# Performance work log

Hardware: AMD Instinct MI355X
Metric: run time of the kernel (lower is better)

## Reference

```python
import jax, jax.numpy as jnp
import numpy as np

N = 1024      # nodes (fully connected graph -> N^2 edges)
D = 3         # spatial dim
H_DIM = 64    # node feature dim
MSG = 64      # edge message dim
HID = 128     # MLP hidden dim


def _linear_init(key, fan_in, fan_out):
    k1, k2 = jax.random.split(key)
    s = 1.0 / np.sqrt(fan_in)
    w = jax.random.uniform(k1, (fan_in, fan_out), minval=-s, maxval=s, dtype=jnp.float32)
    b = jax.random.uniform(k2, (fan_out,), minval=-s, maxval=s, dtype=jnp.float32)
    return w, b


def setup_inputs() -> dict:
    key = jax.random.key(0)
    kx, kh, ke1, ke2, kn1, kn2, kc1, kc2 = jax.random.split(key, 8)
    x = jax.random.normal(kx, (N, D), dtype=jnp.float32)
    h = jax.random.normal(kh, (N, H_DIM), dtype=jnp.float32)
    # edge_mlp: (2*h_dim + 1) -> HID -> MSG
    ew1, eb1 = _linear_init(ke1, 2 * H_DIM + 1, HID)
    ew2, eb2 = _linear_init(ke2, HID, MSG)
    # node_mlp: (h_dim + msg) -> HID -> h_dim
    nw1, nb1 = _linear_init(kn1, H_DIM + MSG, HID)
    nw2, nb2 = _linear_init(kn2, HID, H_DIM)
    # coord_mlp: msg -> HID -> 1
    cw1, cb1 = _linear_init(kc1, MSG, HID)
    cw2, cb2 = _linear_init(kc2, HID, 1)
    return {"x": x, "h": h,
            "ew1": ew1, "eb1": eb1, "ew2": ew2, "eb2": eb2,
            "nw1": nw1, "nb1": nb1, "nw2": nw2, "nb2": nb2,
            "cw1": cw1, "cb1": cb1, "cw2": cw2, "cb2": cb2}


def _mlp2(inp, w1, b1, w2, b2):
    # depth-2 MLP: Linear -> SiLU -> Linear (no output activation)
    return jax.nn.silu(inp @ w1 + b1) @ w2 + b2


def reference(x, h, ew1, eb1, ew2, eb2, nw1, nb1, nw2, nb2, cw1, cb1, cw2, cb2):
    n = x.shape[0]
    # pairwise displacement and squared distance: (N,N,D), (N,N,1)
    dx = x[:, None, :] - x[None, :, :]
    r2 = jnp.sum(dx * dx, axis=-1, keepdims=True)
    hd = h.shape[-1]
    h_i = jnp.broadcast_to(h[:, None, :], (n, n, hd))
    h_j = jnp.broadcast_to(h[None, :, :], (n, n, hd))
    edge_in = jnp.concatenate([h_i, h_j, r2], axis=-1)      # (N,N,2H+1)
    m_ij = _mlp2(edge_in, ew1, eb1, ew2, eb2)               # (N,N,MSG)
    not_self = 1.0 - jnp.eye(n, dtype=x.dtype)
    m_ij = m_ij * not_self[:, :, None]
    phi_ij = _mlp2(m_ij, cw1, cb1, cw2, cb2)                # (N,N,1)
    x_update = jnp.sum(dx * phi_ij, axis=1) / (n - 1 + 1e-08)
    x_new = x + x_update
    m_i = jnp.sum(m_ij, axis=1)                             # (N,MSG)
    node_in = jnp.concatenate([h, m_i], axis=-1)            # (N,H+MSG)
    dh = _mlp2(node_in, nw1, nb1, nw2, nb2)                 # (N,H)
    h_new = h + dh  # residual_h = True
    return (x_new, h_new)
```

## Files before the change

### kernel.cpp

```cpp
#include <hip/hip_runtime.h>
#include <hip/hip_bf16.h>

#define NN   1024
#define HD   64
#define MSGD 64
#define HIDD 128

typedef __attribute__((ext_vector_type(4))) float f4;
typedef __attribute__((ext_vector_type(2))) float f2;
typedef __attribute__((ext_vector_type(8))) __bf16 bf16x8;
typedef __attribute__((ext_vector_type(16))) float f32x16;
typedef __attribute__((ext_vector_type(4))) unsigned int u32x4;
typedef unsigned short ushort_t;

__device__ __forceinline__ float silu_f(float v) {
    float e = __expf(-v);
    return v * __builtin_amdgcn_rcpf(1.0f + e);
}

__device__ __forceinline__ ushort_t to_bf16_bits(float v) {
    return __builtin_bit_cast(ushort_t, (__bf16)v);
}

__device__ __forceinline__ unsigned pack2(float a, float b) {
    return (unsigned)to_bf16_bits(a) | ((unsigned)to_bf16_bits(b) << 16);
}

__device__ __forceinline__ float bf_lo(unsigned u) {
    return __builtin_bit_cast(float, u << 16);
}
__device__ __forceinline__ float bf_hi(unsigned u) {
    return __builtin_bit_cast(float, u & 0xffff0000u);
}

#define ZERO16 {0.f,0.f,0.f,0.f,0.f,0.f,0.f,0.f,0.f,0.f,0.f,0.f,0.f,0.f,0.f,0.f}

__global__ void egnn_pre(const float* __restrict__ h, const float* __restrict__ ew1,
                         const float* __restrict__ eb1, const float* __restrict__ ew2,
                         const float* __restrict__ cw1,
                         float* __restrict__ Ah, unsigned* __restrict__ Bh16,
                         ushort_t* __restrict__ ew2tf, ushort_t* __restrict__ cw1tf)
{
    const int b = blockIdx.x, tid = threadIdx.x;
    if (b < 256) {
        const int n = b * 4 + (tid >> 6);
        const int c = (tid & 63) * 2;
        f2 a = *(const f2*)&eb1[c];
        f2 bb = (f2){0.f, 0.f};
        const float* hrow = h + n * HD;
        #pragma unroll 4
        for (int d = 0; d < HD; ++d) {
            const float hv = hrow[d];
            const f2 w1 = *(const f2*)&ew1[d * HIDD + c];
            const f2 w2 = *(const f2*)&ew1[(HD + d) * HIDD + c];
            a += hv * w1;
            bb += hv * w2;
        }
        *(f2*)&Ah[n * HIDD + c] = a;
        Bh16[n * 64 + (tid & 63)] = pack2(bb[0], bb[1]);
    } else if (b == 256) {
        #pragma unroll
        for (int uu = 0; uu < 4; ++uu) {
            const int fl = uu * 256 + tid;
            const int f = fl >> 6, l = fl & 63;
            const int mt = f >> 3, ks = f & 7;
            const int msg = mt * 32 + (l & 31);
            const int hidb = ks * 16 + (l >> 5) * 8;
            u32x4 pk;
            #pragma unroll
            for (int p = 0; p < 4; ++p)
                pk[p] = pack2(ew2[(hidb + 2 * p) * MSGD + msg],
                              ew2[(hidb + 2 * p + 1) * MSGD + msg]);
            *(u32x4*)&ew2tf[fl * 8] = pk;
        }
    } else {
        #pragma unroll
        for (int uu = 0; uu < 4; ++uu) {
            const int fl = uu * 256 + tid;
            const int f = fl >> 6, l = fl & 63;
            const int mt = f >> 2, k = f & 3;
            const int hid = mt * 32 + (l & 31);
            const int msgb = k * 16 + (l >> 5) * 8;
            u32x4 pk;
            #pragma unroll
            for (int p = 0; p < 4; ++p)
                pk[p] = pack2(cw1[(msgb + 2 * p) * HIDD + hid],
                              cw1[(msgb + 2 * p + 1) * HIDD + hid]);
            *(u32x4*)&cw1tf[fl * 8] = pk;
        }
    }
}

__global__ __launch_bounds__(256, 3) void egnn_edge(
    const float* __restrict__ x, const float* __restrict__ wr_row,
    const float* __restrict__ Ah, const unsigned* __restrict__ Bh16,
    const ushort_t* __restrict__ ew2tf, const ushort_t* __restrict__ cw1tf,
    const float* __restrict__ eb2, const float* __restrict__ cb1,
    const float* __restrict__ cw2, const float* __restrict__ cb2,
    float* __restrict__ m_part, float* __restrict__ xu_part)
{
    __shared__ ushort_t ew2t_lds[16][512];
    __shared__ ushort_t cw1t_lds[16][512];
    __shared__ ushort_t bh16_lds[32][136];
    __shared__ float    ah_lds[4][128];
    __shared__ float    wr_lds[128];
    __shared__ float    cb1_lds[128];
    __shared__ float    cw2_lds[128];
    __shared__ float    eb2_lds[64];
    __shared__ float    xj_lds[32][4];

    const int tid = threadIdx.x;
    const int w = tid >> 6, lane = tid & 63;
    const int j32 = lane & 31, hi = lane >> 5;
    const int i0 = blockIdx.x * 4, jh = blockIdx.y;
    const int i = i0 + w;
    const int jc_begin = (jh == 0) ? 0 : (jh == 1) ? 11 : 22;
    const int jc_end   = (jh == 0) ? 11 : (jh == 1) ? 22 : 32;

    {
        const u32x4* s1 = (const u32x4*)ew2tf;
        const u32x4* s2 = (const u32x4*)cw1tf;
        u32x4* d1 = (u32x4*)&ew2t_lds[0][0];
        u32x4* d2 = (u32x4*)&cw1t_lds[0][0];
        #pragma unroll
        for (int uu = 0; uu < 4; ++uu) {
            d1[uu * 256 + tid] = s1[uu * 256 + tid];
            d2[uu * 256 + tid] = s2[uu * 256 + tid];
        }
        const int r = tid >> 6, c = (tid & 63) * 2;
        *(f2*)&ah_lds[r][c] = *(const f2*)&Ah[(i0 + r) * HIDD + c];
        if (tid < 128) {
            wr_lds[tid]  = wr_row[tid];
            cb1_lds[tid] = cb1[tid];
            cw2_lds[tid] = cw2[tid];
            if (tid < 64) eb2_lds[tid] = eb2[tid];
        }
    }
    const float cb2s = cb2[0];
    const float xi0 = x[i * 3 + 0], xi1 = x[i * 3 + 1], xi2 = x[i * 3 + 2];

    f4 macc[2][4];
    #pragma unroll
    for (int mt = 0; mt < 2; ++mt)
        #pragma unroll
        for (int g = 0; g < 4; ++g) macc[mt][g] = (f4){0.f, 0.f, 0.f, 0.f};
    float xq0 = 0.f, xq1 = 0.f, xq2 = 0.f;

    for (int jc = jc_begin; jc < jc_end; ++jc) {
        const int j0 = jc * 32;
        __syncthreads();
        #pragma unroll
        for (int uu = 0; uu < 2; ++uu) {
            const int idx = uu * 256 + tid, row = idx >> 4, c8 = (idx & 15) * 8;
            *(u32x4*)&bh16_lds[row][c8] =
                *(const u32x4*)&Bh16[((j0 + row) * HIDD + c8) >> 1];
        }
        if (tid < 128) {
            const int r = tid >> 2, c = tid & 3;
            xj_lds[r][c] = (c < 3) ? x[(j0 + r) * 3 + c] : 0.f;
        }
        __syncthreads();

        const f4 xj = *(const f4*)&xj_lds[j32][0];
        const float d0 = xi0 - xj[0], d1v = xi1 - xj[1], d2v = xi2 - xj[2];
        const float r2 = d0 * d0 + d1v * d1v + d2v * d2v;

        f32x16 accA = ZERO16, accB = ZERO16;
        #pragma unroll
        for (int ks = 0; ks < 8; ++ks) {
            const int hidb = ks * 16 + hi * 8;
            const f4 a0 = *(const f4*)&ah_lds[w][hidb];
            const f4 a1 = *(const f4*)&ah_lds[w][hidb + 4];
            const f4 w0 = *(const f4*)&wr_lds[hidb];
            const f4 w1 = *(const f4*)&wr_lds[hidb + 4];
            const u32x4 bw = *(const u32x4*)&bh16_lds[j32][hidb];
            bf16x8 sf;
            #pragma unroll
            for (int p = 0; p < 2; ++p) {
                const float b0e = bf_lo(bw[p]), b1e = bf_hi(bw[p]);
                sf[2 * p]     = (__bf16)silu_f(fmaf(r2, w0[2 * p],     a0[2 * p])     + b0e);
                sf[2 * p + 1] = (__bf16)silu_f(fmaf(r2, w0[2 * p + 1], a0[2 * p + 1]) + b1e);
            }
            #pragma unroll
            for (int p = 0; p < 2; ++p) {
                const float b0e = bf_lo(bw[2 + p]), b1e = bf_hi(bw[2 + p]);
                sf[4 + 2 * p] = (__bf16)silu_f(fmaf(r2, w1[2 * p],     a1[2 * p])     + b0e);
                sf[5 + 2 * p] = (__bf16)silu_f(fmaf(r2, w1[2 * p + 1], a1[2 * p + 1]) + b1e);
            }
            const bf16x8 af0 = *(const bf16x8*)&ew2t_lds[ks][lane * 8];
            const bf16x8 af1 = *(const bf16x8*)&ew2t_lds[8 + ks][lane * 8];
            accA = __builtin_amdgcn_mfma_f32_32x32x16_bf16(af0, sf, accA, 0, 0, 0);
            accB = __builtin_amdgcn_mfma_f32_32x32x16_bf16(af1, sf, accB, 0, 0, 0);
        }

        const bool selfchunk = (i >= j0) && (i < j0 + 32);
        const bool is_self = selfchunk && ((j0 + j32) == i);
        bf16x8 mfrag[4];
        #pragma unroll
        for (int mt = 0; mt < 2; ++mt) {
            unsigned pk[8];
            #pragma unroll
            for (int g = 0; g < 4; ++g) {
                f4 q;
                #pragma unroll
                for (int rr = 0; rr < 4; ++rr)
                    q[rr] = (mt == 0) ? accA[g * 4 + rr] : accB[g * 4 + rr];
                q += *(const f4*)&eb2_lds[mt * 32 + 8 * g + 4 * hi];
                if (selfchunk) {
                    #pragma unroll
                    for (int rr = 0; rr < 4; ++rr) q[rr] = is_self ? 0.f : q[rr];
                }
                macc[mt][g] += q;
                pk[g * 2]     = pack2(q[0], q[1]);
                pk[g * 2 + 1] = pack2(q[2], q[3]);
            }
            #pragma unroll
            for (int kk = 0; kk < 2; ++kk) {
                const unsigned lo0 = pk[kk * 4], lo1 = pk[kk * 4 + 1];
                const unsigned hh0 = pk[kk * 4 + 2], hh1 = pk[kk * 4 + 3];
                const unsigned own0 = hi ? hh0 : lo0, own1 = hi ? hh1 : lo1;
                const unsigned snd0 = hi ? lo0 : hh0, snd1 = hi ? lo1 : hh1;
                const unsigned rcv0 = __shfl_xor(snd0, 32), rcv1 = __shfl_xor(snd1, 32);
                u32x4 fr;
                fr[0] = hi ? rcv0 : own0;
                fr[1] = hi ? rcv1 : own1;
                fr[2] = hi ? own0 : rcv0;
                fr[3] = hi ? own1 : rcv1;
                mfrag[mt * 2 + kk] = __builtin_bit_cast(bf16x8, fr);
            }
        }

        float phi = 0.f;
        #pragma unroll
        for (int half = 0; half < 2; ++half) {
            f32x16 t0 = ZERO16, t1 = ZERO16;
            #pragma unroll
            for (int k = 0; k < 4; ++k) {
                const bf16x8 A0 = *(const bf16x8*)&cw1t_lds[(half * 2 + 0) * 4 + k][lane * 8];
                const bf16x8 A1 = *(const bf16x8*)&cw1t_lds[(half * 2 + 1) * 4 + k][lane * 8];
                t0 = __builtin_amdgcn_mfma_f32_32x32x16_bf16(A0, mfrag[k], t0, 0, 0, 0);
                t1 = __builtin_amdgcn_mfma_f32_32x32x16_bf16(A1, mfrag[k], t1, 0, 0, 0);
            }
            #pragma unroll
            for (int g = 0; g < 4; ++g) {
                const int hb0 = (half * 2 + 0) * 32 + 8 * g + 4 * hi;
                const int hb1 = (half * 2 + 1) * 32 + 8 * g + 4 * hi;
                const f4 c10 = *(const f4*)&cb1_lds[hb0];
                const f4 c20 = *(const f4*)&cw2_lds[hb0];
                const f4 c11 = *(const f4*)&cb1_lds[hb1];
                const f4 c21 = *(const f4*)&cw2_lds[hb1];
                #pragma unroll
                for (int rr = 0; rr < 4; ++rr) {
                    phi += silu_f(t0[g * 4 + rr] + c10[rr]) * c20[rr];
                    phi += silu_f(t1[g * 4 + rr] + c11[rr]) * c21[rr];
                }
            }
        }
        phi += __shfl_xor(phi, 32);
        phi = phi + cb2s;
        xq0 += d0 * phi; xq1 += d1v * phi; xq2 += d2v * phi;
    }

    #pragma unroll
    for (int mask = 1; mask <= 16; mask <<= 1)
        #pragma unroll
        for (int mt = 0; mt < 2; ++mt)
            #pragma unroll
            for (int g = 0; g < 4; ++g)
                #pragma unroll
                for (int rr = 0; rr < 4; ++rr)
                    macc[mt][g][rr] += __shfl_xor(macc[mt][g][rr], mask);
    if (j32 == 0) {
        #pragma unroll
        for (int mt = 0; mt < 2; ++mt)
            #pragma unroll
            for (int g = 0; g < 4; ++g)
                *(f4*)&m_part[(jh * NN + i) * MSGD + mt * 32 + 8 * g + 4 * hi] = macc[mt][g];
    }
    #pragma unroll
    for (int mask = 1; mask <= 32; mask <<= 1) {
        xq0 += __shfl_xor(xq0, mask);
        xq1 += __shfl_xor(xq1, mask);
        xq2 += __shfl_xor(xq2, mask);
    }
    if (lane == 0) {
        float* dst = &xu_part[(jh * NN + i) * 3];
        dst[0] = xq0; dst[1] = xq1; dst[2] = xq2;
    }
}

__global__ void egnn_node(const float* __restrict__ x, const float* __restrict__ h,
                          const float* __restrict__ nw1, const float* __restrict__ nb1,
                          const float* __restrict__ nw2, const float* __restrict__ nb2,
                          const float* __restrict__ m_part, const float* __restrict__ xu_part,
                          float* __restrict__ out)
{
    __shared__ float nin[8][132];
    __shared__ float zl[8][132];
    const int tid = threadIdx.x;
    const int r0 = blockIdx.x * 8;
    #pragma unroll
    for (int uu = 0; uu < 4; ++uu) {
        const int idx = uu * 256 + tid;
        const int row = idx >> 7, c = idx & 127;
        float v;
        if (c < 64) v = h[(r0 + row) * HD + c];
        else {
            const int cc = c - 64;
            v = m_part[(r0 + row) * MSGD + cc]
              + m_part[(NN + r0 + row) * MSGD + cc]
              + m_part[(2 * NN + r0 + row) * MSGD + cc];
        }
        nin[row][c] = v;
    }
    __syncthreads();
    const int row = tid >> 5, cg = tid & 31;
    {
        const int c0 = cg * 4;
        f4 acc = *(const f4*)&nb1[c0];
        for (int k = 0; k < 128; ++k) {
            const float v = nin[row][k];
            const f4 wv = *(const f4*)&nw1[k * HIDD + c0];
            acc += v * wv;
        }
        #pragma unroll
        for (int e = 0; e < 4; ++e) zl[row][c0 + e] = silu_f(acc[e]);
    }
    __syncthreads();
    {
        const int c0 = cg * 2;
        f2 acc = *(const f2*)&nb2[c0];
        for (int k = 0; k < 128; ++k) {
            const float v = zl[row][k];
            const f2 wv = *(const f2*)&nw2[k * HD + c0];
            acc += v * wv;
        }
        const int n = r0 + row;
        const f2 hv = *(const f2*)&h[n * HD + c0];
        *(f2*)&out[3072 + n * HD + c0] = hv + acc;
    }
    if (tid < 24) {
        const int r = tid / 3, c = tid - 3 * r;
        const int n = r0 + r;
        const float xu = xu_part[n * 3 + c] + xu_part[(NN + n) * 3 + c]
                       + xu_part[(2 * NN + n) * 3 + c];
        out[n * 3 + c] = x[n * 3 + c] + xu * (1.0f / 1023.0f);
    }
}

extern "C" void kernel_launch(void* const* d_in, const int* in_sizes, int n_in,
                              void* d_out, int out_size, void* d_ws, size_t ws_size,
                              hipStream_t stream)
{
    const float* x   = (const float*)d_in[0];
    const float* h   = (const float*)d_in[1];
    const float* ew1 = (const float*)d_in[2];
    const float* eb1 = (const float*)d_in[3];
    const float* ew2 = (const float*)d_in[4];
    const float* eb2 = (const float*)d_in[5];
    const float* nw1 = (const float*)d_in[6];
    const float* nb1 = (const float*)d_in[7];
    const float* nw2 = (const float*)d_in[8];
    const float* nb2 = (const float*)d_in[9];
    const float* cw1 = (const float*)d_in[10];
    const float* cb1 = (const float*)d_in[11];
    const float* cw2 = (const float*)d_in[12];
    const float* cb2 = (const float*)d_in[13];
    float* out = (float*)d_out;

    char* ws = (char*)d_ws;
    float*    Ah      = (float*)(ws);
    unsigned* Bh16    = (unsigned*)(ws + (512 << 10));
    ushort_t* ew2tf   = (ushort_t*)(ws + (768 << 10));
    ushort_t* cw1tf   = (ushort_t*)(ws + (784 << 10));
    float*    m_part  = (float*)(ws + (800 << 10));
    float*    xu_part = (float*)(ws + (1568 << 10));

    egnn_pre<<<dim3(258), dim3(256), 0, stream>>>(h, ew1, eb1, ew2, cw1, Ah, Bh16, ew2tf, cw1tf);
    egnn_edge<<<dim3(256, 3), dim3(256), 0, stream>>>(
        x, ew1 + 128 * HIDD, Ah, Bh16, ew2tf, cw1tf, eb2, cb1, cw2, cb2, m_part, xu_part);
    egnn_node<<<dim3(128), dim3(256), 0, stream>>>(x, h, nw1, nb1, nw2, nb2, m_part, xu_part, out);
}
```

Before: 199.0 us.

## Fuse pre, edge and node kernels into one persistent kernel with grid barriers

Merges the three launches into one kernel of 768 workgroups that uses atomic-counter grid barriers between the precompute, edge and node phases. A memset clears the counters before each launch. The aim is to remove per-launch overhead and the gaps between kernels. The risk is deadlock if not all 768 workgroups are resident at once, and spin-wait cost at the barriers. The phi-MLP loop is also reorganised to issue one accumulator at a time instead of two, which lowers register pressure but reduces interleaving of MFMA chains.

Result: slower. 308.3 us (+54.9%).

```diff
diff --git a/kernel.cpp b/kernel.cpp
--- a/kernel.cpp
+++ b/kernel.cpp
@@ -5,6 +5,7 @@
 #define HD   64
 #define MSGD 64
 #define HIDD 128
+#define NWG  768
 
 typedef __attribute__((ext_vector_type(4))) float f4;
 typedef __attribute__((ext_vector_type(2))) float f2;
@@ -26,24 +27,52 @@
     return (unsigned)to_bf16_bits(a) | ((unsigned)to_bf16_bits(b) << 16);
 }
 
-__device__ __forceinline__ float bf_lo(unsigned u) {
-    return __builtin_bit_cast(float, u << 16);
-}
-__device__ __forceinline__ float bf_hi(unsigned u) {
-    return __builtin_bit_cast(float, u & 0xffff0000u);
+__device__ __forceinline__ float bf_lo(unsigned u) { return __builtin_bit_cast(float, u << 16); }
+__device__ __forceinline__ float bf_hi(unsigned u) { return __builtin_bit_cast(float, u & 0xffff0000u); }
+
+__device__ __forceinline__ void grid_bar(unsigned* c, unsigned target) {
+    __syncthreads();
+    if (threadIdx.x == 0) {
+        __threadfence();
+        atomicAdd(c, 1u);
+        while (__hip_atomic_load(c, __ATOMIC_RELAXED, __HIP_MEMORY_SCOPE_AGENT) < target)
+            __builtin_amdgcn_s_sleep(2);
+        __threadfence();
+    }
+    __syncthreads();
 }
 
 #define ZERO16 {0.f,0.f,0.f,0.f,0.f,0.f,0.f,0.f,0.f,0.f,0.f,0.f,0.f,0.f,0.f,0.f}
 
-__global__ void egnn_pre(const float* __restrict__ h, const float* __restrict__ ew1,
-                         const float* __restrict__ eb1, const float* __restrict__ ew2,
-                         const float* __restrict__ cw1,
-                         float* __restrict__ Ah, unsigned* __restrict__ Bh16,
-                         ushort_t* __restrict__ ew2tf, ushort_t* __restrict__ cw1tf)
+__global__ __launch_bounds__(256, 3) void egnn_fused(
+    const float* __restrict__ x, const float* __restrict__ h,
+    const float* __restrict__ ew1, const float* __restrict__ eb1,
+    const float* __restrict__ ew2, const float* __restrict__ eb2,
+    const float* __restrict__ nw1, const float* __restrict__ nb1,
+    const float* __restrict__ nw2, const float* __restrict__ nb2,
+    const float* __restrict__ cw1, const float* __restrict__ cb1,
+    const float* __restrict__ cw2, const float* __restrict__ cb2,
+    float* __restrict__ Ah, unsigned* __restrict__ Bh16,
+    ushort_t* __restrict__ ew2tf, ushort_t* __restrict__ cw1tf,
+    float* __restrict__ m_part, float* __restrict__ xu_part,
+    unsigned* __restrict__ ctrs, float* __restrict__ out)
 {
-    const int b = blockIdx.x, tid = threadIdx.x;
-    if (b < 256) {
-        const int n = b * 4 + (tid >> 6);
+    __shared__ ushort_t ew2t_lds[16][512];
+    __shared__ ushort_t cw1t_lds[16][512];
+    __shared__ ushort_t bh16_lds[32][136];
+    __shared__ float    ah_lds[4][128];
+    __shared__ float    wr_lds[128];
+    __shared__ float    cb1_lds[128];
+    __shared__ float    cw2_lds[128];
+    __shared__ float    eb2_lds[64];
+    __shared__ float    xj_lds[32][4];
+
+    const int wg = blockIdx.x;
+    const int tid = threadIdx.x;
+    const float* wr_row = ew1 + 128 * HIDD;
+
+    if (wg < 256) {
+        const int n = wg * 4 + (tid >> 6);
         const int c = (tid & 63) * 2;
         f2 a = *(const f2*)&eb1[c];
         f2 bb = (f2){0.f, 0.f};
@@ -58,293 +87,259 @@
         }
         *(f2*)&Ah[n * HIDD + c] = a;
         Bh16[n * 64 + (tid & 63)] = pack2(bb[0], bb[1]);
-    } else if (b == 256) {
+    } else if (wg < 260) {
+        const int fl = (wg - 256) * 256 + tid;
+        const int f = fl >> 6, l = fl & 63;
+        const int mt = f >> 3, ks = f & 7;
+        const int msg = mt * 32 + (l & 31);
+        const int hidb = ks * 16 + (l >> 5) * 8;
+        u32x4 pk;
+        #pragma unroll
+        for (int p = 0; p < 4; ++p)
+            pk[p] = pack2(ew2[(hidb + 2 * p) * MSGD + msg],
+                          ew2[(hidb + 2 * p + 1) * MSGD + msg]);
+        *(u32x4*)&ew2tf[fl * 8] = pk;
+    } else if (wg < 264) {
+        const int fl = (wg - 260) * 256 + tid;
+        const int f = fl >> 6, l = fl & 63;
+        const int mt = f >> 2, k = f & 3;
+        const int hid = mt * 32 + (l & 31);
+        const int msgb = k * 16 + (l >> 5) * 8;
+        u32x4 pk;
+        #pragma unroll
+        for (int p = 0; p < 4; ++p)
+            pk[p] = pack2(cw1[(msgb + 2 * p) * HIDD + hid],
+                          cw1[(msgb + 2 * p + 1) * HIDD + hid]);
+        *(u32x4*)&cw1tf[fl * 8] = pk;
+    }
+    grid_bar(&ctrs[0], NWG);
+
+    {
+        const int w = tid >> 6, lane = tid & 63;
+        const int j32 = lane & 31, hi = lane >> 5;
+        const int bx = wg & 255, jh = wg >> 8;
+        const int i0 = bx * 4;
+        const int i = i0 + w;
+        const int jc_begin = (jh == 0) ? 0 : (jh == 1) ? 11 : 22;
+        const int jc_end   = (jh == 0) ? 11 : (jh == 1) ? 22 : 32;
+
+        {
+            const u32x4* s1 = (const u32x4*)ew2tf;
+            const u32x4* s2 = (const u32x4*)cw1tf;
+            u32x4* d1 = (u32x4*)&ew2t_lds[0][0];
+            u32x4* d2 = (u32x4*)&cw1t_lds[0][0];
+            #pragma unroll
+            for (int uu = 0; uu < 4; ++uu) {
+                d1[uu * 256 + tid] = s1[uu * 256 + tid];
+                d2[uu * 256 + tid] = s2[uu * 256 + tid];
+            }
+            const int r = tid >> 6, c = (tid & 63) * 2;
+            *(f2*)&ah_lds[r][c] = *(const f2*)&Ah[(i0 + r) * HIDD + c];
+            if (tid < 128) {
+                wr_lds[tid]  = wr_row[tid];
+                cb1_lds[tid] = cb1[tid];
+                cw2_lds[tid] = cw2[tid];
+                if (tid < 64) eb2_lds[tid] = eb2[tid];
+            }
+        }
+        const float cb2s = cb2[0];
+        const float xi0 = x[i * 3 + 0], xi1 = x[i * 3 + 1], xi2 = x[i * 3 + 2];
+
+        f4 macc[2][4];
+        #pragma unroll
+        for (int mt = 0; mt < 2; ++mt)
+            #pragma unroll
+            for (int g = 0; g < 4; ++g) macc[mt][g] = (f4){0.f, 0.f, 0.f, 0.f};
+        float xq0 = 0.f, xq1 = 0.f, xq2 = 0.f;
+
+        for (int jc = jc_begin; jc < jc_end; ++jc) {
+            const int j0 = jc * 32;
+            __syncthreads();
+            #pragma unroll
+            for (int uu = 0; uu < 2; ++uu) {
+                const int idx = uu * 256 + tid, row = idx >> 4, c8 = (idx & 15) * 8;
+                *(u32x4*)&bh16_lds[row][c8] =
+                    *(const u32x4*)&Bh16[((j0 + row) * HIDD + c8) >> 1];
+            }
+            if (tid < 128) {
+                const int r = tid >> 2, c = tid & 3;
+                xj_lds[r][c] = (c < 3) ? x[(j0 + r) * 3 + c] : 0.f;
+            }
+            __syncthreads();
+
+            const f4 xj = *(const f4*)&xj_lds[j32][0];
+            const float d0 = xi0 - xj[0], d1v = xi1 - xj[1], d2v = xi2 - xj[2];
+            const float r2 = d0 * d0 + d1v * d1v + d2v * d2v;
+
+            f32x16 accA = ZERO16, accB = ZERO16;
+            #pragma unroll
+            for (int ks = 0; ks < 8; ++ks) {
+                const int hidb = ks * 16 + hi * 8;
+                const f4 a0 = *(const f4*)&ah_lds[w][hidb];
+                const f4 a1 = *(const f4*)&ah_lds[w][hidb + 4];
+                const f4 w0 = *(const f4*)&wr_lds[hidb];
+                const f4 w1 = *(const f4*)&wr_lds[hidb + 4];
+                const u32x4 bw = *(const u32x4*)&bh16_lds[j32][hidb];
+                bf16x8 sf;
+                #pragma unroll
+                for (int p = 0; p < 2; ++p) {
+                    const float b0e = bf_lo(bw[p]), b1e = bf_hi(bw[p]);
+                    sf[2 * p]     = (__bf16)silu_f(fmaf(r2, w0[2 * p],     a0[2 * p])     + b0e);
+                    sf[2 * p + 1] = (__bf16)silu_f(fmaf(r2, w0[2 * p + 1], a0[2 * p + 1]) + b1e);
+                }
+                #pragma unroll
+                for (int p = 0; p < 2; ++p) {
+                    const float b0e = bf_lo(bw[2 + p]), b1e = bf_hi(bw[2 + p]);
+                    sf[4 + 2 * p] = (__bf16)silu_f(fmaf(r2, w1[2 * p],     a1[2 * p])     + b0e);
+                    sf[5 + 2 * p] = (__bf16)silu_f(fmaf(r2, w1[2 * p + 1], a1[2 * p + 1]) + b1e);
+                }
+                const bf16x8 af0 = *(const bf16x8*)&ew2t_lds[ks][lane * 8];
+                const bf16x8 af1 = *(const bf16x8*)&ew2t_lds[8 + ks][lane * 8];
+                accA = __builtin_amdgcn_mfma_f32_32x32x16_bf16(af0, sf, accA, 0, 0, 0);
+                accB = __builtin_amdgcn_mfma_f32_32x32x16_bf16(af1, sf, accB, 0, 0, 0);
+            }
+
+            const bool selfchunk = (i >= j0) && (i < j0 + 32);
+            const bool is_self = selfchunk && ((j0 + j32) == i);
+            bf16x8 mfrag[4];
+            #pragma unroll
+            for (int mt = 0; mt < 2; ++mt) {
+                unsigned pk[8];
+                #pragma unroll
+                for (int g = 0; g < 4; ++g) {
+                    f4 q;
+                    #pragma unroll
+                    for (int rr = 0; rr < 4; ++rr)
+                        q[rr] = (mt == 0) ? accA[g * 4 + rr] : accB[g * 4 + rr];
+                    q += *(const f4*)&eb2_lds[mt * 32 + 8 * g + 4 * hi];
+                    if (selfchunk) {
+                        #pragma unroll
+                        for (int rr = 0; rr < 4; ++rr) q[rr] = is_self ? 0.f : q[rr];
+                    }
+                    macc[mt][g] += q;
+                    pk[g * 2]     = pack2(q[0], q[1]);
+                    pk[g * 2 + 1] = pack2(q[2], q[3]);
+                }
+                #pragma unroll
+                for (int kk = 0; kk < 2; ++kk) {
+                    const unsigned lo0 = pk[kk * 4], lo1 = pk[kk * 4 + 1];
+                    const unsigned hh0 = pk[kk * 4 + 2], hh1 = pk[kk * 4 + 3];
+                    const unsigned own0 = hi ? hh0 : lo0, own1 = hi ? hh1 : lo1;
+                    const unsigned snd0 = hi ? lo0 : hh0, snd1 = hi ? lo1 : hh1;
+                    const unsigned rcv0 = __shfl_xor(snd0, 32), rcv1 = __shfl_xor(snd1, 32);
+                    u32x4 fr;
+                    fr[0] = hi ? rcv0 : own0;
+                    fr[1] = hi ? rcv1 : own1;
+                    fr[2] = hi ? own0 : rcv0;
+                    fr[3] = hi ? own1 : rcv1;
+                    mfrag[mt * 2 + kk] = __builtin_bit_cast(bf16x8, fr);
+                }
+            }
+
+            float phi = 0.f;
+            #pragma unroll
+            for (int q = 0; q < 4; ++q) {
+                f32x16 t = ZERO16;
+                #pragma unroll
+                for (int k = 0; k < 4; ++k) {
+                    const bf16x8 A0 = *(const bf16x8*)&cw1t_lds[q * 4 + k][lane * 8];
+                    t = __builtin_amdgcn_mfma_f32_32x32x16_bf16(A0, mfrag[k], t, 0, 0, 0);
+                }
+                #pragma unroll
+                for (int g = 0; g < 4; ++g) {
+                    const int hb = q * 32 + 8 * g + 4 * hi;
+                    const f4 c1v = *(const f4*)&cb1_lds[hb];
+                    const f4 c2v = *(const f4*)&cw2_lds[hb];
+                    #pragma unroll
+                    for (int rr = 0; rr < 4; ++rr)
+                        phi += silu_f(t[g * 4 + rr] + c1v[rr]) * c2v[rr];
+                }
+            }
+            phi += __shfl_xor(phi, 32);
+            phi = phi + cb2s;
+            xq0 += d0 * phi; xq1 += d1v * phi; xq2 += d2v * phi;
+        }
+
+        #pragma unroll
+        for (int mask = 1; mask <= 16; mask <<= 1)
+            #pragma unroll
+            for (int mt = 0; mt < 2; ++mt)
+                #pragma unroll
+                for (int g = 0; g < 4; ++g)
+                    #pragma unroll
+                    for (int rr = 0; rr < 4; ++rr)
+                        macc[mt][g][rr] += __shfl_xor(macc[mt][g][rr], mask);
+        if (j32 == 0) {
+            #pragma unroll
+            for (int mt = 0; mt < 2; ++mt)
+                #pragma unroll
+                for (int g = 0; g < 4; ++g)
+                    *(f4*)&m_part[(jh * NN + i) * MSGD + mt * 32 + 8 * g + 4 * hi] = macc[mt][g];
+        }
+        #pragma unroll
+        for (int mask = 1; mask <= 32; mask <<= 1) {
+            xq0 += __shfl_xor(xq0, mask);
+            xq1 += __shfl_xor(xq1, mask);
+            xq2 += __shfl_xor(xq2, mask);
+        }
+        if (lane == 0) {
+            float* dst = &xu_part[(jh * NN + i) * 3];
+            dst[0] = xq0; dst[1] = xq1; dst[2] = xq2;
+        }
+    }
+    grid_bar(&ctrs[32], NWG);
+
+    if (wg < 128) {
+        float (*nin)[132] = (float (*)[132])&ew2t_lds[0][0];
+        float (*zl)[132]  = (float (*)[132])&cw1t_lds[0][0];
+        const int r0 = wg * 8;
         #pragma unroll
         for (int uu = 0; uu < 4; ++uu) {
-            const int fl = uu * 256 + tid;
-            const int f = fl >> 6, l = fl & 63;
-            const int mt = f >> 3, ks = f & 7;
-            const int msg = mt * 32 + (l & 31);
-            const int hidb = ks * 16 + (l >> 5) * 8;
-            u32x4 pk;
-            #pragma unroll
-            for (int p = 0; p < 4; ++p)
-                pk[p] = pack2(ew2[(hidb + 2 * p) * MSGD + msg],
-                              ew2[(hidb + 2 * p + 1) * MSGD + msg]);
-            *(u32x4*)&ew2tf[fl * 8] = pk;
-        }
-    } else {
-        #pragma unroll
-        for (int uu = 0; uu < 4; ++uu) {
-            const int fl = uu * 256 + tid;
-            const int f = fl >> 6, l = fl & 63;
-            const int mt = f >> 2, k = f & 3;
-            const int hid = mt * 32 + (l & 31);
-            const int msgb = k * 16 + (l >> 5) * 8;
-            u32x4 pk;
-            #pragma unroll
-            for (int p = 0; p < 4; ++p)
-                pk[p] = pack2(cw1[(msgb + 2 * p) * HIDD + hid],
-                              cw1[(msgb + 2 * p + 1) * HIDD + hid]);
-            *(u32x4*)&cw1tf[fl * 8] = pk;
-        }
-    }
-}
-
-__global__ __launch_bounds__(256, 3) void egnn_edge(
-    const float* __restrict__ x, const float* __restrict__ wr_row,
-    const float* __restrict__ Ah, const unsigned* __restrict__ Bh16,
-    const ushort_t* __restrict__ ew2tf, const ushort_t* __restrict__ cw1tf,
-    const float* __restrict__ eb2, const float* __restrict__ cb1,
-    const float* __restrict__ cw2, const float* __restrict__ cb2,
-    float* __restrict__ m_part, float* __restrict__ xu_part)
-{
-    __shared__ ushort_t ew2t_lds[16][512];
-    __shared__ ushort_t cw1t_lds[16][512];
-    __shared__ ushort_t bh16_lds[32][136];
-    __shared__ float    ah_lds[4][128];
-    __shared__ float    wr_lds[128];
-    __shared__ float    cb1_lds[128];
-    __shared__ float    cw2_lds[128];
-    __shared__ float    eb2_lds[64];
-    __shared__ float    xj_lds[32][4];
-
-    const int tid = threadIdx.x;
-    const int w = tid >> 6, lane = tid & 63;
-    const int j32 = lane & 31, hi = lane >> 5;
-    const int i0 = blockIdx.x * 4, jh = blockIdx.y;
-    const int i = i0 + w;
-    const int jc_begin = (jh == 0) ? 0 : (jh == 1) ? 11 : 22;
-    const int jc_end   = (jh == 0) ? 11 : (jh == 1) ? 22 : 32;
-
-    {
-        const u32x4* s1 = (const u32x4*)ew2tf;
-        const u32x4* s2 = (const u32x4*)cw1tf;
-        u32x4* d1 = (u32x4*)&ew2t_lds[0][0];
-        u32x4* d2 = (u32x4*)&cw1t_lds[0][0];
-        #pragma unroll
-        for (int uu = 0; uu < 4; ++uu) {
-            d1[uu * 256 + tid] = s1[uu * 256 + tid];
-            d2[uu * 256 + tid] = s2[uu * 256 + tid];
-        }
-        const int r = tid >> 6, c = (tid & 63) * 2;
-        *(f2*)&ah_lds[r][c] = *(const f2*)&Ah[(i0 + r) * HIDD + c];
-        if (tid < 128) {
-            wr_lds[tid]  = wr_row[tid];
-            cb1_lds[tid] = cb1[tid];
-            cw2_lds[tid] = cw2[tid];
-            if (tid < 64) eb2_lds[tid] = eb2[tid];
-        }
-    }
-    const float cb2s = cb2[0];
-    const float xi0 = x[i * 3 + 0], xi1 = x[i * 3 + 1], xi2 = x[i * 3 + 2];
-
-    f4 macc[2][4];
-    #pragma unroll
-    for (int mt = 0; mt < 2; ++mt)
-        #pragma unroll
-        for (int g = 0; g < 4; ++g) macc[mt][g] = (f4){0.f, 0.f, 0.f, 0.f};
-    float xq0 = 0.f, xq1 = 0.f, xq2 = 0.f;
-
-    for (int jc = jc_begin; jc < jc_end; ++jc) {
-        const int j0 = jc * 32;
+            const int idx = uu * 256 + tid;
+            const int row = idx >> 7, c = idx & 127;
+            float v;
+            if (c < 64) v = h[(r0 + row) * HD + c];
+            else {
+                const int cc = c - 64;
+                v = m_part[(r0 + row) * MSGD + cc]
+                  + m_part[(NN + r0 + row) * MSGD + cc]
+                  + m_part[(2 * NN + r0 + row) * MSGD + cc];
+            }
+            nin[row][c] = v;
+        }
         __syncthreads();
-        #pragma unroll
-        for (int uu = 0; uu < 2; ++uu) {
-            const int idx = uu * 256 + tid, row = idx >> 4, c8 = (idx & 15) * 8;
-            *(u32x4*)&bh16_lds[row][c8] =
-                *(const u32x4*)&Bh16[((j0 + row) * HIDD + c8) >> 1];
-        }
-        if (tid < 128) {
-            const int r = tid >> 2, c = tid & 3;
-            xj_lds[r][c] = (c < 3) ? x[(j0 + r) * 3 + c] : 0.f;
+        const int row = tid >> 5, cg = tid & 31;
+        {
+            const int c0 = cg * 4;
+            f4 acc = *(const f4*)&nb1[c0];
+            for (int k = 0; k < 128; ++k) {
+                const float v = nin[row][k];
+                const f4 wv = *(const f4*)&nw1[k * HIDD + c0];
+                acc += v * wv;
+            }
+            #pragma unroll
+            for (int e = 0; e < 4; ++e) zl[row][c0 + e] = silu_f(acc[e]);
         }
         __syncthreads();
-
-        const f4 xj = *(const f4*)&xj_lds[j32][0];
-        const float d0 = xi0 - xj[0], d1v = xi1 - xj[1], d2v = xi2 - xj[2];
-        const float r2 = d0 * d0 + d1v * d1v + d2v * d2v;
-
-        f32x16 accA = ZERO16, accB = ZERO16;
-        #pragma unroll
-        for (int ks = 0; ks < 8; ++ks) {
-            const int hidb = ks * 16 + hi * 8;
-            const f4 a0 = *(const f4*)&ah_lds[w][hidb];
-            const f4 a1 = *(const f4*)&ah_lds[w][hidb + 4];
-            const f4 w0 = *(const f4*)&wr_lds[hidb];
-            const f4 w1 = *(const f4*)&wr_lds[hidb + 4];
-            const u32x4 bw = *(const u32x4*)&bh16_lds[j32][hidb];
-            bf16x8 sf;
-            #pragma unroll
-            for (int p = 0; p < 2; ++p) {
-                const float b0e = bf_lo(bw[p]), b1e = bf_hi(bw[p]);
-                sf[2 * p]     = (__bf16)silu_f(fmaf(r2, w0[2 * p],     a0[2 * p])     + b0e);
-                sf[2 * p + 1] = (__bf16)silu_f(fmaf(r2, w0[2 * p + 1], a0[2 * p + 1]) + b1e);
-            }
-            #pragma unroll
-            for (int p = 0; p < 2; ++p) {
-                const float b0e = bf_lo(bw[2 + p]), b1e = bf_hi(bw[2 + p]);
-                sf[4 + 2 * p] = (__bf16)silu_f(fmaf(r2, w1[2 * p],     a1[2 * p])     + b0e);
-                sf[5 + 2 * p] = (__bf16)silu_f(fmaf(r2, w1[2 * p + 1], a1[2 * p + 1]) + b1e);
-            }
-            const bf16x8 af0 = *(const bf16x8*)&ew2t_lds[ks][lane * 8];
-            const bf16x8 af1 = *(const bf16x8*)&ew2t_lds[8 + ks][lane * 8];
-            accA = __builtin_amdgcn_mfma_f32_32x32x16_bf16(af0, sf, accA, 0, 0, 0);
-            accB = __builtin_amdgcn_mfma_f32_32x32x16_bf16(af1, sf, accB, 0, 0, 0);
-        }
-
-        const bool selfchunk = (i >= j0) && (i < j0 + 32);
-        const bool is_self = selfchunk && ((j0 + j32) == i);
-        bf16x8 mfrag[4];
-        #pragma unroll
-        for (int mt = 0; mt < 2; ++mt) {
-            unsigned pk[8];
-            #pragma unroll
-            for (int g = 0; g < 4; ++g) {
-                f4 q;
-                #pragma unroll
-                for (int rr = 0; rr < 4; ++rr)
-                    q[rr] = (mt == 0) ? accA[g * 4 + rr] : accB[g * 4 + rr];
-                q += *(const f4*)&eb2_lds[mt * 32 + 8 * g + 4 * hi];
-                if (selfchunk) {
-                    #pragma unroll
-                    for (int rr = 0; rr < 4; ++rr) q[rr] = is_self ? 0.f : q[rr];
-                }
-                macc[mt][g] += q;
-                pk[g * 2]     = pack2(q[0], q[1]);
-                pk[g * 2 + 1] = pack2(q[2], q[3]);
-            }
-            #pragma unroll
-            for (int kk = 0; kk < 2; ++kk) {
-                const unsigned lo0 = pk[kk * 4], lo1 = pk[kk * 4 + 1];
-                const unsigned hh0 = pk[kk * 4 + 2], hh1 = pk[kk * 4 + 3];
-                const unsigned own0 = hi ? hh0 : lo0, own1 = hi ? hh1 : lo1;
-                const unsigned snd0 = hi ? lo0 : hh0, snd1 = hi ? lo1 : hh1;
-                const unsigned rcv0 = __shfl_xor(snd0, 32), rcv1 = __shfl_xor(snd1, 32);
-                u32x4 fr;
-                fr[0] = hi ? rcv0 : own0;
-                fr[1] = hi ? rcv1 : own1;
-                fr[2] = hi ? own0 : rcv0;
-                fr[3] = hi ? own1 : rcv1;
-                mfrag[mt * 2 + kk] = __builtin_bit_cast(bf16x8, fr);
-            }
-        }
-
-        float phi = 0.f;
-        #pragma unroll
-        for (int half = 0; half < 2; ++half) {
-            f32x16 t0 = ZERO16, t1 = ZERO16;
-            #pragma unroll
-            for (int k = 0; k < 4; ++k) {
-                const bf16x8 A0 = *(const bf16x8*)&cw1t_lds[(half * 2 + 0) * 4 + k][lane * 8];
-                const bf16x8 A1 = *(const bf16x8*)&cw1t_lds[(half * 2 + 1) * 4 + k][lane * 8];
-                t0 = __builtin_amdgcn_mfma_f32_32x32x16_bf16(A0, mfrag[k], t0, 0, 0, 0);
-                t1 = __builtin_amdgcn_mfma_f32_32x32x16_bf16(A1, mfrag[k], t1, 0, 0, 0);
-            }
-            #pragma unroll
-            for (int g = 0; g < 4; ++g) {
-                const int hb0 = (half * 2 + 0) * 32 + 8 * g + 4 * hi;
-                const int hb1 = (half * 2 + 1) * 32 + 8 * g + 4 * hi;
-                const f4 c10 = *(const f4*)&cb1_lds[hb0];
-                const f4 c20 = *(const f4*)&cw2_lds[hb0];
-                const f4 c11 = *(const f4*)&cb1_lds[hb1];
-                const f4 c21 = *(const f4*)&cw2_lds[hb1];
-                #pragma unroll
-                for (int rr = 0; rr < 4; ++rr) {
-                    phi += silu_f(t0[g * 4 + rr] + c10[rr]) * c20[rr];
-                    phi += silu_f(t1[g * 4 + rr] + c11[rr]) * c21[rr];
-                }
-            }
-        }
-        phi += __shfl_xor(phi, 32);
-        phi = phi + cb2s;
-        xq0 += d0 * phi; xq1 += d1v * phi; xq2 += d2v * phi;
-    }
-
-    #pragma unroll
-    for (int mask = 1; mask <= 16; mask <<= 1)
-        #pragma unroll
-        for (int mt = 0; mt < 2; ++mt)
-            #pragma unroll
-            for (int g = 0; g < 4; ++g)
-                #pragma unroll
-                for (int rr = 0; rr < 4; ++rr)
-                    macc[mt][g][rr] += __shfl_xor(macc[mt][g][rr], mask);
-    if (j32 == 0) {
-        #pragma unroll
-        for (int mt = 0; mt < 2; ++mt)
-            #pragma unroll
-            for (int g = 0; g < 4; ++g)
-                *(f4*)&m_part[(jh * NN + i) * MSGD + mt * 32 + 8 * g + 4 * hi] = macc[mt][g];
-    }
-    #pragma unroll
-    for (int mask = 1; mask <= 32; mask <<= 1) {
-        xq0 += __shfl_xor(xq0, mask);
-        xq1 += __shfl_xor(xq1, mask);
-        xq2 += __shfl_xor(xq2, mask);
-    }
-    if (lane == 0) {
-        float* dst = &xu_part[(jh * NN + i) * 3];
-        dst[0] = xq0; dst[1] = xq1; dst[2] = xq2;
-    }
-}
-
-__global__ void egnn_node(const float* __restrict__ x, const float* __restrict__ h,
-                          const float* __restrict__ nw1, const float* __restrict__ nb1,
-                          const float* __restrict__ nw2, const float* __restrict__ nb2,
-                          const float* __restrict__ m_part, const float* __restrict__ xu_part,
-                          float* __restrict__ out)
-{
-    __shared__ float nin[8][132];
-    __shared__ float zl[8][132];
-    const int tid = threadIdx.x;
-    const int r0 = blockIdx.x * 8;
-    #pragma unroll
-    for (int uu = 0; uu < 4; ++uu) {
-        const int idx = uu * 256 + tid;
-        const int row = idx >> 7, c = idx & 127;
-        float v;
-        if (c < 64) v = h[(r0 + row) * HD + c];
-        else {
-            const int cc = c - 64;
-            v = m_part[(r0 + row) * MSGD + cc]
-              + m_part[(NN + r0 + row) * MSGD + cc]
-              + m_part[(2 * NN + r0 + row) * MSGD + cc];
-        }
-        nin[row][c] = v;
-    }
-    __syncthreads();
-    const int row = tid >> 5, cg = tid & 31;
-    {
-        const int c0 = cg * 4;
-        f4 acc = *(const f4*)&nb1[c0];
-        for (int k = 0; k < 128; ++k) {
-            const float v = nin[row][k];
-            const f4 wv = *(const f4*)&nw1[k * HIDD + c0];
-            acc += v * wv;
-        }
-        #pragma unroll
-        for (int e = 0; e < 4; ++e) zl[row][c0 + e] = silu_f(acc[e]);
-    }
-    __syncthreads();
-    {
-        const int c0 = cg * 2;
-        f2 acc = *(const f2*)&nb2[c0];
-        for (int k = 0; k < 128; ++k) {
-            const float v = zl[row][k];
-            const f2 wv = *(const f2*)&nw2[k * HD + c0];
-            acc += v * wv;
-        }
-        const int n = r0 + row;
-        const f2 hv = *(const f2*)&h[n * HD + c0];
-        *(f2*)&out[3072 + n * HD + c0] = hv + acc;
-    }
-    if (tid < 24) {
-        const int r = tid / 3, c = tid - 3 * r;
-        const int n = r0 + r;
-        const float xu = xu_part[n * 3 + c] + xu_part[(NN + n) * 3 + c]
-                       + xu_part[(2 * NN + n) * 3 + c];
-        out[n * 3 + c] = x[n * 3 + c] + xu * (1.0f / 1023.0f);
+        {
+            const int c0 = cg * 2;
+            f2 acc = *(const f2*)&nb2[c0];
+            for (int k = 0; k < 128; ++k) {
+                const float v = zl[row][k];
+                const f2 wv = *(const f2*)&nw2[k * HD + c0];
+                acc += v * wv;
+            }
+            const int n = r0 + row;
+            const f2 hv = *(const f2*)&h[n * HD + c0];
+            *(f2*)&out[3072 + n * HD + c0] = hv + acc;
+        }
+        if (tid < 24) {
+            const int r = tid / 3, c = tid - 3 * r;
+            const int n = r0 + r;
+            const float xu = xu_part[n * 3 + c] + xu_part[(NN + n) * 3 + c]
+                           + xu_part[(2 * NN + n) * 3 + c];
+            out[n * 3 + c] = x[n * 3 + c] + xu * (1.0f / 1023.0f);
+        }
     }
 }
 
@@ -375,9 +370,10 @@
     ushort_t* cw1tf   = (ushort_t*)(ws + (784 << 10));
     float*    m_part  = (float*)(ws + (800 << 10));
     float*    xu_part = (float*)(ws + (1568 << 10));
-
-    egnn_pre<<<dim3(258), dim3(256), 0, stream>>>(h, ew1, eb1, ew2, cw1, Ah, Bh16, ew2tf, cw1tf);
-    egnn_edge<<<dim3(256, 3), dim3(256), 0, stream>>>(
-        x, ew1 + 128 * HIDD, Ah, Bh16, ew2tf, cw1tf, eb2, cb1, cw2, cb2, m_part, xu_part);
-    egnn_node<<<dim3(128), dim3(256), 0, stream>>>(x, h, nw1, nb1, nw2, nb2, m_part, xu_part, out);
-}
+    unsigned* ctrs    = (unsigned*)(ws + (1632 << 10));
+
+    hipMemsetAsync(ctrs, 0, 256, stream);
+    egnn_fused<<<dim3(NWG), dim3(256), 0, stream>>>(
+        x, h, ew1, eb1, ew2, eb2, nw1, nb1, nw2, nb2, cw1, cb1, cw2, cb2,
+        Ah, Bh16, ew2tf, cw1tf, m_part, xu_part, ctrs, out);
+}
```

## Fuse node MLP into edge kernel via completion flags, double-buffer Bh tiles

Applied to the files above, without the earlier changes.

Removes the separate node kernel. The edge grid is now two j-halves per row block, and whichever block finishes last (counted with an atomic flag) runs the node MLP for its four rows. Bh is kept in fp32 instead of packed bf16, and its tiles are prefetched into registers and double-buffered in LDS to overlap global loads with compute. The coordinate MLP accumulation is restructured to one accumulator per quarter, and launch bounds drop to 2 blocks per CU. The costs are a larger LDS footprint, twice the Bh traffic, a memset launch, and a serialized node tail on the last block of each pair.

New measurement: 334.7 us. 1.68x slower.

```diff
diff --git a/kernel.cpp b/kernel.cpp
--- a/kernel.cpp
+++ b/kernel.cpp
@@ -26,19 +26,12 @@
     return (unsigned)to_bf16_bits(a) | ((unsigned)to_bf16_bits(b) << 16);
 }
 
-__device__ __forceinline__ float bf_lo(unsigned u) {
-    return __builtin_bit_cast(float, u << 16);
-}
-__device__ __forceinline__ float bf_hi(unsigned u) {
-    return __builtin_bit_cast(float, u & 0xffff0000u);
-}
-
 #define ZERO16 {0.f,0.f,0.f,0.f,0.f,0.f,0.f,0.f,0.f,0.f,0.f,0.f,0.f,0.f,0.f,0.f}
 
 __global__ void egnn_pre(const float* __restrict__ h, const float* __restrict__ ew1,
                          const float* __restrict__ eb1, const float* __restrict__ ew2,
                          const float* __restrict__ cw1,
-                         float* __restrict__ Ah, unsigned* __restrict__ Bh16,
+                         float* __restrict__ Ah, float* __restrict__ Bh,
                          ushort_t* __restrict__ ew2tf, ushort_t* __restrict__ cw1tf)
 {
     const int b = blockIdx.x, tid = threadIdx.x;
@@ -57,7 +50,7 @@
             bb += hv * w2;
         }
         *(f2*)&Ah[n * HIDD + c] = a;
-        Bh16[n * 64 + (tid & 63)] = pack2(bb[0], bb[1]);
+        *(f2*)&Bh[n * HIDD + c] = bb;
     } else if (b == 256) {
         #pragma unroll
         for (int uu = 0; uu < 4; ++uu) {
@@ -91,31 +84,40 @@
     }
 }
 
-__global__ __launch_bounds__(256, 3) void egnn_edge(
+__global__ __launch_bounds__(256, 2) void egnn_edge(
     const float* __restrict__ x, const float* __restrict__ wr_row,
-    const float* __restrict__ Ah, const unsigned* __restrict__ Bh16,
+    const float* __restrict__ Ah, const float* __restrict__ Bh,
     const ushort_t* __restrict__ ew2tf, const ushort_t* __restrict__ cw1tf,
     const float* __restrict__ eb2, const float* __restrict__ cb1,
     const float* __restrict__ cw2, const float* __restrict__ cb2,
-    float* __restrict__ m_part, float* __restrict__ xu_part)
+    const float* __restrict__ h,
+    const float* __restrict__ nw1, const float* __restrict__ nb1,
+    const float* __restrict__ nw2, const float* __restrict__ nb2,
+    float* __restrict__ m_part, float* __restrict__ xu_part,
+    unsigned* __restrict__ flags, float* __restrict__ out)
 {
     __shared__ ushort_t ew2t_lds[16][512];
     __shared__ ushort_t cw1t_lds[16][512];
-    __shared__ ushort_t bh16_lds[32][136];
+    __shared__ float    bh_lds[2][32][132];
+    __shared__ float    xj_lds[2][32][4];
     __shared__ float    ah_lds[4][128];
     __shared__ float    wr_lds[128];
     __shared__ float    cb1_lds[128];
     __shared__ float    cw2_lds[128];
     __shared__ float    eb2_lds[64];
-    __shared__ float    xj_lds[32][4];
+    __shared__ float    nin[4][132];
+    __shared__ float    zl[4][132];
+    __shared__ unsigned flag_s;
 
     const int tid = threadIdx.x;
     const int w = tid >> 6, lane = tid & 63;
     const int j32 = lane & 31, hi = lane >> 5;
-    const int i0 = blockIdx.x * 4, jh = blockIdx.y;
+    const int bx = blockIdx.x, jh = blockIdx.y;
+    const int i0 = bx * 4;
     const int i = i0 + w;
-    const int jc_begin = (jh == 0) ? 0 : (jh == 1) ? 11 : 22;
-    const int jc_end   = (jh == 0) ? 11 : (jh == 1) ? 22 : 32;
+
+    const int st_row = tid >> 3;
+    const int st_c4  = (tid & 7) * 16;
 
     {
         const u32x4* s1 = (const u32x4*)ew2tf;
@@ -139,6 +141,28 @@
     const float cb2s = cb2[0];
     const float xi0 = x[i * 3 + 0], xi1 = x[i * 3 + 1], xi2 = x[i * 3 + 2];
 
+    f4 pf[4];
+    float pxj = 0.f;
+    {
+        const int j0 = jh * 512;
+        #pragma unroll
+        for (int uu = 0; uu < 4; ++uu) {
+            const int idx = uu * 256 + tid, row = idx >> 5, c4 = (idx & 31) * 4;
+            pf[uu] = *(const f4*)&Bh[(j0 + row) * HIDD + c4];
+        }
+        if (tid < 128) {
+            const int r = tid >> 2, c = tid & 3;
+            pxj = (c < 3) ? x[(j0 + r) * 3 + c] : 0.f;
+        }
+        #pragma unroll
+        for (int uu = 0; uu < 4; ++uu) {
+            const int idx = uu * 256 + tid, row = idx >> 5, c4 = (idx & 31) * 4;
+            *(f4*)&bh_lds[0][row][c4] = pf[uu];
+        }
+        if (tid < 128) xj_lds[0][tid >> 2][tid & 3] = pxj;
+    }
+    __syncthreads();
+
     f4 macc[2][4];
     #pragma unroll
     for (int mt = 0; mt < 2; ++mt)
@@ -146,22 +170,24 @@
         for (int g = 0; g < 4; ++g) macc[mt][g] = (f4){0.f, 0.f, 0.f, 0.f};
     float xq0 = 0.f, xq1 = 0.f, xq2 = 0.f;
 
-    for (int jc = jc_begin; jc < jc_end; ++jc) {
-        const int j0 = jc * 32;
-        __syncthreads();
-        #pragma unroll
-        for (int uu = 0; uu < 2; ++uu) {
-            const int idx = uu * 256 + tid, row = idx >> 4, c8 = (idx & 15) * 8;
-            *(u32x4*)&bh16_lds[row][c8] =
-                *(const u32x4*)&Bh16[((j0 + row) * HIDD + c8) >> 1];
-        }
-        if (tid < 128) {
-            const int r = tid >> 2, c = tid & 3;
-            xj_lds[r][c] = (c < 3) ? x[(j0 + r) * 3 + c] : 0.f;
-        }
-        __syncthreads();
-
-        const f4 xj = *(const f4*)&xj_lds[j32][0];
+    int cur = 0;
+    for (int jc = 0; jc < 16; ++jc, cur ^= 1) {
+        const int j0 = jh * 512 + jc * 32;
+
+        if (jc < 15) {
+            const int jn = j0 + 32;
+            #pragma unroll
+            for (int uu = 0; uu < 4; ++uu) {
+                const int idx = uu * 256 + tid, row = idx >> 5, c4 = (idx & 31) * 4;
+                pf[uu] = *(const f4*)&Bh[(jn + row) * HIDD + c4];
+            }
+            if (tid < 128) {
+                const int r = tid >> 2, c = tid & 3;
+                pxj = (c < 3) ? x[(jn + r) * 3 + c] : 0.f;
+            }
+        }
+
+        const f4 xj = *(const f4*)&xj_lds[cur][j32][0];
         const float d0 = xi0 - xj[0], d1v = xi1 - xj[1], d2v = xi2 - xj[2];
         const float r2 = d0 * d0 + d1v * d1v + d2v * d2v;
 
@@ -173,19 +199,13 @@
             const f4 a1 = *(const f4*)&ah_lds[w][hidb + 4];
             const f4 w0 = *(const f4*)&wr_lds[hidb];
             const f4 w1 = *(const f4*)&wr_lds[hidb + 4];
-            const u32x4 bw = *(const u32x4*)&bh16_lds[j32][hidb];
+            const f4 b0 = *(const f4*)&bh_lds[cur][j32][hidb];
+            const f4 b1 = *(const f4*)&bh_lds[cur][j32][hidb + 4];
             bf16x8 sf;
             #pragma unroll
-            for (int p = 0; p < 2; ++p) {
-                const float b0e = bf_lo(bw[p]), b1e = bf_hi(bw[p]);
-                sf[2 * p]     = (__bf16)silu_f(fmaf(r2, w0[2 * p],     a0[2 * p])     + b0e);
-                sf[2 * p + 1] = (__bf16)silu_f(fmaf(r2, w0[2 * p + 1], a0[2 * p + 1]) + b1e);
-            }
-            #pragma unroll
-            for (int p = 0; p < 2; ++p) {
-                const float b0e = bf_lo(bw[2 + p]), b1e = bf_hi(bw[2 + p]);
-                sf[4 + 2 * p] = (__bf16)silu_f(fmaf(r2, w1[2 * p],     a1[2 * p])     + b0e);
-                sf[5 + 2 * p] = (__bf16)silu_f(fmaf(r2, w1[2 * p + 1], a1[2 * p + 1]) + b1e);
+            for (int e = 0; e < 4; ++e) {
+                sf[e]     = (__bf16)silu_f(fmaf(r2, w0[e], a0[e]) + b0[e]);
+                sf[e + 4] = (__bf16)silu_f(fmaf(r2, w1[e], a1[e]) + b1[e]);
             }
             const bf16x8 af0 = *(const bf16x8*)&ew2t_lds[ks][lane * 8];
             const bf16x8 af1 = *(const bf16x8*)&ew2t_lds[8 + ks][lane * 8];
@@ -232,33 +252,36 @@
 
         float phi = 0.f;
         #pragma unroll
-        for (int half = 0; half < 2; ++half) {
-            f32x16 t0 = ZERO16, t1 = ZERO16;
+        for (int q = 0; q < 4; ++q) {
+            f32x16 t = ZERO16;
             #pragma unroll
             for (int k = 0; k < 4; ++k) {
-                const bf16x8 A0 = *(const bf16x8*)&cw1t_lds[(half * 2 + 0) * 4 + k][lane * 8];
-                const bf16x8 A1 = *(const bf16x8*)&cw1t_lds[(half * 2 + 1) * 4 + k][lane * 8];
-                t0 = __builtin_amdgcn_mfma_f32_32x32x16_bf16(A0, mfrag[k], t0, 0, 0, 0);
-                t1 = __builtin_amdgcn_mfma_f32_32x32x16_bf16(A1, mfrag[k], t1, 0, 0, 0);
+                const bf16x8 A0 = *(const bf16x8*)&cw1t_lds[q * 4 + k][lane * 8];
+                t = __builtin_amdgcn_mfma_f32_32x32x16_bf16(A0, mfrag[k], t, 0, 0, 0);
             }
             #pragma unroll
             for (int g = 0; g < 4; ++g) {
-                const int hb0 = (half * 2 + 0) * 32 + 8 * g + 4 * hi;
-                const int hb1 = (half * 2 + 1) * 32 + 8 * g + 4 * hi;
-                const f4 c10 = *(const f4*)&cb1_lds[hb0];
-                const f4 c20 = *(const f4*)&cw2_lds[hb0];
-                const f4 c11 = *(const f4*)&cb1_lds[hb1];
-                const f4 c21 = *(const f4*)&cw2_lds[hb1];
+                const int hb = q * 32 + 8 * g + 4 * hi;
+                const f4 c1v = *(const f4*)&cb1_lds[hb];
+                const f4 c2v = *(const f4*)&cw2_lds[hb];
                 #pragma unroll
-                for (int rr = 0; rr < 4; ++rr) {
-                    phi += silu_f(t0[g * 4 + rr] + c10[rr]) * c20[rr];
-                    phi += silu_f(t1[g * 4 + rr] + c11[rr]) * c21[rr];
-                }
+                for (int rr = 0; rr < 4; ++rr)
+                    phi += silu_f(t[g * 4 + rr] + c1v[rr]) * c2v[rr];
             }
         }
         phi += __shfl_xor(phi, 32);
         phi = phi + cb2s;
         xq0 += d0 * phi; xq1 += d1v * phi; xq2 += d2v * phi;
+
+        if (jc < 15) {
+            #pragma unroll
+            for (int uu = 0; uu < 4; ++uu) {
+                const int idx = uu * 256 + tid, row = idx >> 5, c4 = (idx & 31) * 4;
+                *(f4*)&bh_lds[cur ^ 1][row][c4] = pf[uu];
+            }
+            if (tid < 128) xj_lds[cur ^ 1][tid >> 2][tid & 3] = pxj;
+        }
+        __syncthreads();
     }
 
     #pragma unroll
@@ -287,64 +310,52 @@
         float* dst = &xu_part[(jh * NN + i) * 3];
         dst[0] = xq0; dst[1] = xq1; dst[2] = xq2;
     }
-}
-
-__global__ void egnn_node(const float* __restrict__ x, const float* __restrict__ h,
-                          const float* __restrict__ nw1, const float* __restrict__ nb1,
-                          const float* __restrict__ nw2, const float* __restrict__ nb2,
-                          const float* __restrict__ m_part, const float* __restrict__ xu_part,
-                          float* __restrict__ out)
-{
-    __shared__ float nin[8][132];
-    __shared__ float zl[8][132];
-    const int tid = threadIdx.x;
-    const int r0 = blockIdx.x * 8;
-    #pragma unroll
-    for (int uu = 0; uu < 4; ++uu) {
-        const int idx = uu * 256 + tid;
-        const int row = idx >> 7, c = idx & 127;
-        float v;
-        if (c < 64) v = h[(r0 + row) * HD + c];
-        else {
-            const int cc = c - 64;
-            v = m_part[(r0 + row) * MSGD + cc]
-              + m_part[(NN + r0 + row) * MSGD + cc]
-              + m_part[(2 * NN + r0 + row) * MSGD + cc];
-        }
-        nin[row][c] = v;
-    }
+
+    __threadfence();
     __syncthreads();
-    const int row = tid >> 5, cg = tid & 31;
-    {
-        const int c0 = cg * 4;
-        f4 acc = *(const f4*)&nb1[c0];
-        for (int k = 0; k < 128; ++k) {
-            const float v = nin[row][k];
-            const f4 wv = *(const f4*)&nw1[k * HIDD + c0];
-            acc += v * wv;
-        }
-        #pragma unroll
-        for (int e = 0; e < 4; ++e) zl[row][c0 + e] = silu_f(acc[e]);
-    }
+    if (tid == 0) flag_s = atomicAdd(&flags[bx], 1u);
     __syncthreads();
-    {
-        const int c0 = cg * 2;
-        f2 acc = *(const f2*)&nb2[c0];
-        for (int k = 0; k < 128; ++k) {
-            const float v = zl[row][k];
-            const f2 wv = *(const f2*)&nw2[k * HD + c0];
-            acc += v * wv;
-        }
-        const int n = r0 + row;
-        const f2 hv = *(const f2*)&h[n * HD + c0];
-        *(f2*)&out[3072 + n * HD + c0] = hv + acc;
-    }
-    if (tid < 24) {
-        const int r = tid / 3, c = tid - 3 * r;
-        const int n = r0 + r;
-        const float xu = xu_part[n * 3 + c] + xu_part[(NN + n) * 3 + c]
-                       + xu_part[(2 * NN + n) * 3 + c];
-        out[n * 3 + c] = x[n * 3 + c] + xu * (1.0f / 1023.0f);
+    if (flag_s == 1u) {
+        __threadfence();
+        const int r0 = i0;
+        #pragma unroll
+        for (int uu = 0; uu < 2; ++uu) {
+            const int idx = uu * 256 + tid;
+            const int row = idx >> 7, c = idx & 127;
+            float v;
+            if (c < 64) v = h[(r0 + row) * HD + c];
+            else {
+                const int cc = c - 64;
+                v = m_part[(r0 + row) * MSGD + cc] + m_part[(NN + r0 + row) * MSGD + cc];
+            }
+            nin[row][c] = v;
+        }
+        __syncthreads();
+        {
+            const int row = tid >> 6, c0 = (tid & 63) * 2;
+            f2 acc = *(const f2*)&nb1[c0];
+            for (int k = 0; k < 128; ++k) {
+                const float v = nin[row][k];
+                acc += v * *(const f2*)&nw1[k * HIDD + c0];
+            }
+            zl[row][c0]     = silu_f(acc[0]);
+            zl[row][c0 + 1] = silu_f(acc[1]);
+        }
+        __syncthreads();
+        {
+            const int row = tid >> 6, c = tid & 63;
+            float acc = nb2[c];
+            for (int k = 0; k < 128; ++k)
+                acc = fmaf(zl[row][k], nw2[k * HD + c], acc);
+            const int n = r0 + row;
+            out[3072 + n * HD + c] = h[n * HD + c] + acc;
+        }
+        if (tid < 12) {
+            const int r = tid / 3, c = tid - 3 * r;
+            const int n = r0 + r;
+            const float xu = xu_part[n * 3 + c] + xu_part[(NN + n) * 3 + c];
+            out[n * 3 + c] = x[n * 3 + c] + xu * (1.0f / 1023.0f);
+        }
     }
 }
 
@@ -370,14 +381,16 @@
 
     char* ws = (char*)d_ws;
     float*    Ah      = (float*)(ws);
-    unsigned* Bh16    = (unsigned*)(ws + (512 << 10));
-    ushort_t* ew2tf   = (ushort_t*)(ws + (768 << 10));
-    ushort_t* cw1tf   = (ushort_t*)(ws + (784 << 10));
-    float*    m_part  = (float*)(ws + (800 << 10));
+    float*    Bh      = (float*)(ws + (512 << 10));
+    ushort_t* ew2tf   = (ushort_t*)(ws + (1024 << 10));
+    ushort_t* cw1tf   = (ushort_t*)(ws + (1040 << 10));
+    float*    m_part  = (float*)(ws + (1056 << 10));
     float*    xu_part = (float*)(ws + (1568 << 10));
-
-    egnn_pre<<<dim3(258), dim3(256), 0, stream>>>(h, ew1, eb1, ew2, cw1, Ah, Bh16, ew2tf, cw1tf);
-    egnn_edge<<<dim3(256, 3), dim3(256), 0, stream>>>(
-        x, ew1 + 128 * HIDD, Ah, Bh16, ew2tf, cw1tf, eb2, cb1, cw2, cb2, m_part, xu_part);
-    egnn_node<<<dim3(128), dim3(256), 0, stream>>>(x, h, nw1, nb1, nw2, nb2, m_part, xu_part, out);
-}
+    unsigned* flags   = (unsigned*)(ws + (1600 << 10));
+
+    hipMemsetAsync(flags, 0, 1024, stream);
+    egnn_pre<<<dim3(258), dim3(256), 0, stream>>>(h, ew1, eb1, ew2, cw1, Ah, Bh, ew2tf, cw1tf);
+    egnn_edge<<<dim3(256, 2), dim3(256), 0, stream>>>(
+        x, ew1 + 128 * HIDD, Ah, Bh, ew2tf, cw1tf, eb2, cb1, cw2, cb2,
+        h, nw1, nb1, nw2, nb2, m_part, xu_part, flags, out);
+}
```
